# Kernel optimization log

Hardware: AMD Instinct MI355X
Metric: run time of the kernel (lower is better)

The kernel has to match this reference:

```python
import jax, jax.numpy as jnp
import numpy as np

B, T, D, H = 2, 2048, 1024, 16
HD = D // H            # head dim = 64
WINDOW = 512           # sliding-window size
EPS = 1e-6
ROPE_BASE = 10000.0


def setup_inputs() -> dict:
    key = jax.random.key(0)
    ks = jax.random.split(key, 5)
    s = 0.02  # init scale for dense kernels
    return {
        "x": jax.random.normal(ks[0], (B, T, D), jnp.float32),
        "Wq": jax.random.normal(ks[1], (D, D), jnp.float32) * s,
        "Wk": jax.random.normal(ks[2], (D, D), jnp.float32) * s,
        "Wv": jax.random.normal(ks[3], (D, D), jnp.float32) * s,
        "Wo": jax.random.normal(ks[4], (D, D), jnp.float32) * s,
        "q_scale": jnp.ones((HD,), jnp.float32),
        "k_scale": jnp.ones((HD,), jnp.float32),
        "sink_logit": jnp.zeros((H,), jnp.float32),
    }


def _rmsnorm(x, scale):
    # x: [..., HD]
    var = jnp.mean(jnp.square(x), axis=-1, keepdims=True)
    return x * jax.lax.rsqrt(var + EPS) * scale


def _rope(x):
    # x: [B, H, T, HD]; standard rotate-half RoPE over the full head dim
    half = HD // 2
    inv_freq = 1.0 / (ROPE_BASE ** (jnp.arange(0, HD, 2, dtype=jnp.float32) / HD))  # [half]
    t = jnp.arange(T, dtype=jnp.float32)
    freqs = t[:, None] * inv_freq[None, :]                # [T, half]
    emb = jnp.concatenate([freqs, freqs], axis=-1)        # [T, HD]
    cos = jnp.cos(emb)[None, None]                        # [1,1,T,HD]
    sin = jnp.sin(emb)[None, None]
    x1, x2 = x[..., :half], x[..., half:]
    rot = jnp.concatenate([-x2, x1], axis=-1)
    return x * cos + rot * sin


def reference(x, Wq, Wk, Wv, Wo, q_scale, k_scale, sink_logit):
    # projections -> [B, T, H, HD]
    q = (x @ Wq).reshape(B, T, H, HD)
    k = (x @ Wk).reshape(B, T, H, HD)
    v = (x @ Wv).reshape(B, T, H, HD)
    # QK RMSNorm over head dim
    q = _rmsnorm(q, q_scale)
    k = _rmsnorm(k, k_scale)
    # -> [B, H, T, HD], then RoPE
    q = _rope(q.transpose(0, 2, 1, 3))
    k = _rope(k.transpose(0, 2, 1, 3))
    v = v.transpose(0, 2, 1, 3)
    # causal sliding-window mask
    idx = jnp.arange(T)
    rel = idx[None, :] - idx[:, None]                     # key - query
    mask = ((rel <= 0) & (rel > -WINDOW))[None, None]     # [1,1,T,T]
    scale = HD ** (-0.5)
    scores = jnp.einsum('bhtd,bhsd->bhts', q, k) * scale
    scores = jnp.where(mask, scores, -jnp.inf)
    # sink-augmented softmax: append per-head sink logit to denominator
    sink = jnp.broadcast_to(sink_logit.reshape(1, H, 1, 1), (B, H, T, 1))
    aug = jnp.concatenate([scores.astype(jnp.float32), sink.astype(jnp.float32)], axis=-1)
    weights = jax.nn.softmax(aug, axis=-1)[..., :T].astype(scores.dtype)
    out = jnp.einsum('bhts,bhsd->bhtd', weights, v)
    out = out.transpose(0, 2, 1, 3).reshape(B, T, D)
    return out @ Wo
```

## Files before the change

### kernel.cpp

```cpp
#include <hip/hip_runtime.h>
#include <math.h>

#define CB 2
#define CT 2048
#define CD 1024
#define CH 16
#define CHD 64
#define CWINDOW 512

typedef __bf16 bf16x8 __attribute__((ext_vector_type(8)));
typedef float floatx4 __attribute__((ext_vector_type(4)));

__device__ __forceinline__ unsigned short f2bf(float f) {
  union { float f; unsigned int u; } v;
  v.f = f;
  unsigned int u = v.u;
  u += 0x7fffu + ((u >> 16) & 1u);
  return (unsigned short)(u >> 16);
}
__device__ __forceinline__ float bf2f(unsigned int h) {
  union { unsigned int u; float f; } v;
  v.u = h << 16;
  return v.f;
}

__global__ __launch_bounds__(256) void cvt_all(const float* __restrict__ x,
                                               const float* __restrict__ Wq,
                                               const float* __restrict__ Wk,
                                               const float* __restrict__ Wv,
                                               const float* __restrict__ Wo,
                                               unsigned short* __restrict__ xb,
                                               unsigned short* __restrict__ WqT,
                                               unsigned short* __restrict__ WkT,
                                               unsigned short* __restrict__ WvT,
                                               unsigned short* __restrict__ WoT) {
  const int z = blockIdx.z;
  if (z < 4) {
    const float* W = z == 0 ? Wq : z == 1 ? Wk : z == 2 ? Wv : Wo;
    unsigned short* Wt = z == 0 ? WqT : z == 1 ? WkT : z == 2 ? WvT : WoT;
    __shared__ float tile[64][65];
    const int k0 = blockIdx.x * 64, n0 = blockIdx.y * 64;
    const int c = threadIdx.x & 63, r4 = threadIdx.x >> 6;
#pragma unroll
    for (int i = 0; i < 16; ++i) {
      int r = i * 4 + r4;
      tile[r][c] = W[(size_t)(k0 + r) * CD + n0 + c];
    }
    __syncthreads();
#pragma unroll
    for (int i = 0; i < 16; ++i) {
      int r = i * 4 + r4;
      Wt[(size_t)(n0 + r) * CD + k0 + c] = f2bf(tile[c][r]);
    }
  } else {
    const int idx = (z - 4) * 256 + blockIdx.y * 16 + blockIdx.x;
    const int i = idx * 256 + threadIdx.x;
    float4 a = ((const float4*)x)[i * 2];
    float4 b = ((const float4*)x)[i * 2 + 1];
    uint4 o;
    o.x = (unsigned int)f2bf(a.x) | ((unsigned int)f2bf(a.y) << 16);
    o.y = (unsigned int)f2bf(a.z) | ((unsigned int)f2bf(a.w) << 16);
    o.z = (unsigned int)f2bf(b.x) | ((unsigned int)f2bf(b.y) << 16);
    o.w = (unsigned int)f2bf(b.z) | ((unsigned int)f2bf(b.w) << 16);
    ((uint4*)xb)[i] = o;
  }
}

__device__ __forceinline__ void async16(const unsigned short* g, unsigned short* l) {
  __builtin_amdgcn_global_load_lds(
      (const __attribute__((address_space(1))) unsigned int*)g,
      (__attribute__((address_space(3))) unsigned int*)l, 16, 0, 0);
}

template <int MODE, int BM>
__device__ __forceinline__ void mfma_gemm_body(const unsigned short* __restrict__ A,
                                               const unsigned short* __restrict__ Bt,
                                               void* __restrict__ Cout,
                                               const float* __restrict__ scale,
                                               float oscale) {
  constexpr int K = CD;
  constexpr int MT = BM / 32;
  __shared__ unsigned short As[BM * 32];
  __shared__ unsigned short Bs[128 * 32];
  const int tid = threadIdx.x;
  const int wave = tid >> 6, lane = tid & 63;
  const int m0 = blockIdx.x * BM, n0 = blockIdx.y * 128;
  const int mq = (wave & 1) * (BM / 2), nq = (wave >> 1) * 64;

  floatx4 acc[MT][4] = {};
  const int srow = lane >> 2;
  const int skc = (lane & 3) * 8;
  const int fr = lane & 15;
  const int fk = (lane >> 4) * 8;

  for (int k0 = 0; k0 < K; k0 += 32) {
    __syncthreads();
#pragma unroll
    for (int it = 0; it < BM / 64; ++it) {
      const int sub = wave * (BM / 64) + it;
      const int row = sub * 16 + srow;
      async16(A + (size_t)(m0 + row) * K + k0 + skc, &As[sub * 512]);
    }
#pragma unroll
    for (int it = 0; it < 2; ++it) {
      const int sub = wave * 2 + it;
      const int row = sub * 16 + srow;
      async16(Bt + (size_t)(n0 + row) * K + k0 + skc, &Bs[sub * 512]);
    }
    __syncthreads();
    bf16x8 af[MT], bg[4];
#pragma unroll
    for (int mt = 0; mt < MT; ++mt)
      af[mt] = *(const bf16x8*)&As[(mq + mt * 16 + fr) * 32 + fk];
#pragma unroll
    for (int nt = 0; nt < 4; ++nt)
      bg[nt] = *(const bf16x8*)&Bs[(nq + nt * 16 + fr) * 32 + fk];
#pragma unroll
    for (int mt = 0; mt < MT; ++mt)
#pragma unroll
      for (int nt = 0; nt < 4; ++nt)
        acc[mt][nt] = __builtin_amdgcn_mfma_f32_16x16x32_bf16(af[mt], bg[nt], acc[mt][nt], 0, 0, 0);
  }

  if (MODE == 1) {
    const int c = lane & 15, g = lane >> 4;
    const int hh = (n0 + nq) >> 6;
    const float kf = -0.2878231366242557f;
    const float inv0 = __expf((float)c * kf);
    const float inv1 = __expf((float)(16 + c) * kf);
    float sc[4];
#pragma unroll
    for (int nt = 0; nt < 4; ++nt) sc[nt] = scale[nt * 16 + c];
#pragma unroll
    for (int mt = 0; mt < MT; ++mt) {
#pragma unroll
      for (int i = 0; i < 4; ++i) {
        const int m = m0 + mq + mt * 16 + g * 4 + i;
        const int b = m >> 11, t = m & (CT - 1);
        float v0 = acc[mt][0][i], v1 = acc[mt][1][i];
        float v2 = acc[mt][2][i], v3 = acc[mt][3][i];
        float ss = v0 * v0 + v1 * v1 + v2 * v2 + v3 * v3;
#pragma unroll
        for (int off = 8; off > 0; off >>= 1) ss += __shfl_xor(ss, off);
        const float rs = rsqrtf(ss * (1.0f / 64.0f) + 1e-6f);
        v0 *= rs * sc[0];
        v1 *= rs * sc[1];
        v2 *= rs * sc[2];
        v3 *= rs * sc[3];
        const float tf = (float)t;
        const float a0 = tf * inv0, a1 = tf * inv1;
        const float s0 = __sinf(a0), c0 = __cosf(a0);
        const float s1 = __sinf(a1), c1 = __cosf(a1);
        unsigned short* dst = (unsigned short*)Cout + ((size_t)(b * CH + hh) * CT + t) * CHD;
        dst[c] = f2bf((v0 * c0 - v2 * s0) * oscale);
        dst[16 + c] = f2bf((v1 * c1 - v3 * s1) * oscale);
        dst[32 + c] = f2bf((v2 * c0 + v0 * s0) * oscale);
        dst[48 + c] = f2bf((v3 * c1 + v1 * s1) * oscale);
      }
    }
  } else {
#pragma unroll
    for (int mt = 0; mt < MT; ++mt) {
#pragma unroll
      for (int nt = 0; nt < 4; ++nt) {
        const int col = n0 + nq + nt * 16 + (lane & 15);
        if (MODE == 2) {
          const int mb = m0 + mq + mt * 16 + (lane >> 4) * 4;
          const int b = mb >> 11, t = mb & (CT - 1);
          const int h = col >> 6, d = col & 63;
          ushort4 o;
          o.x = f2bf(acc[mt][nt][0]);
          o.y = f2bf(acc[mt][nt][1]);
          o.z = f2bf(acc[mt][nt][2]);
          o.w = f2bf(acc[mt][nt][3]);
          *(ushort4*)&((unsigned short*)Cout)[((size_t)(b * CH + h) * CHD + d) * CT + t] = o;
        } else {
#pragma unroll
          for (int i = 0; i < 4; ++i) {
            const int m = m0 + mq + mt * 16 + (lane >> 4) * 4 + i;
            ((float*)Cout)[(size_t)m * CD + col] = acc[mt][nt][i];
          }
        }
      }
    }
  }
}

__global__ __launch_bounds__(256, 3) void gemm_qkv_mfma(const unsigned short* __restrict__ xb,
                                                        const unsigned short* __restrict__ WqT,
                                                        const unsigned short* __restrict__ WkT,
                                                        const unsigned short* __restrict__ WvT,
                                                        unsigned short* __restrict__ Qh,
                                                        unsigned short* __restrict__ Kh,
                                                        unsigned short* __restrict__ Vt,
                                                        const float* __restrict__ q_scale,
                                                        const float* __restrict__ k_scale) {
  if (blockIdx.z == 2) {
    mfma_gemm_body<2, 128>(xb, WvT, Vt, nullptr, 1.0f);
  } else if (blockIdx.z == 0) {
    mfma_gemm_body<1, 128>(xb, WqT, Qh, q_scale, 0.125f);
  } else {
    mfma_gemm_body<1, 128>(xb, WkT, Kh, k_scale, 1.0f);
  }
}

__global__ __launch_bounds__(256, 3) void gemm_out_mfma(const unsigned short* __restrict__ AO,
                                                        const unsigned short* __restrict__ WoT,
                                                        float* __restrict__ out) {
  mfma_gemm_body<0, 64>(AO, WoT, out, nullptr, 1.0f);
}

__device__ __forceinline__ bf16x8 frag64(const unsigned short* base, int row, int ks, int lane) {
  const int phys = (((ks << 2) + (lane >> 4)) ^ (lane & 7)) << 3;
  return *(const bf16x8*)&base[(row << 6) + phys];
}

__global__ __launch_bounds__(256, 2) void attn_mfma(const unsigned short* __restrict__ Qh,
                                                    const unsigned short* __restrict__ Kh,
                                                    const unsigned short* __restrict__ Vt,
                                                    const float* __restrict__ sink_logit,
                                                    unsigned short* __restrict__ AO) {
  __shared__ unsigned short Qs[128 * 64];
  __shared__ unsigned short Ks[64 * 64];
  __shared__ unsigned short Vs[64 * 64];
  __shared__ unsigned short Ps[128 * 72];

  const int tid = threadIdx.x;
  const int w = tid >> 6, lane = tid & 63;
  const int qb = blockIdx.x, bh = blockIdx.y;
  const int b = bh >> 4, h = bh & 15;
  const int q0 = qb * 128;
  const unsigned short* Qb = Qh + (size_t)bh * CT * CHD;
  const unsigned short* Kb = Kh + (size_t)bh * CT * CHD;
  const unsigned short* Vb = Vt + (size_t)bh * CHD * CT;

  const int l7 = lane & 7, l8 = lane >> 3;
  const int sx8 = (l7 ^ l8) * 8;

#pragma unroll
  for (int s = 0; s < 4; ++s) {
    const int slab = w * 4 + s;
    async16(Qb + (size_t)(q0 + slab * 8 + l8) * CHD + sx8, &Qs[slab * 512]);
  }
  __syncthreads();
  bf16x8 qf[2][2];
#pragma unroll
  for (int nt = 0; nt < 2; ++nt)
#pragma unroll
    for (int ks = 0; ks < 2; ++ks)
      qf[nt][ks] = frag64(Qs, w * 32 + nt * 16 + (lane & 15), ks, lane);

  floatx4 acc[4][2] = {};
  float lsum[2] = {0.f, 0.f};
  const int qw = q0 + w * 32;

  const int kb_lo = (qb >= 4) ? (qb * 2 - 8) : 0;
  const int kb_hi = qb * 2 + 1;
  for (int kb = kb_lo; kb <= kb_hi; ++kb) {
    __syncthreads();
#pragma unroll
    for (int s = 0; s < 2; ++s) {
      const int slab = w * 2 + s;
      const int row = slab * 8 + l8;
      async16(Kb + (size_t)(kb * 64 + row) * CHD + sx8, &Ks[slab * 512]);
      async16(Vb + (size_t)row * CT + kb * 64 + sx8, &Vs[slab * 512]);
    }
    __syncthreads();

    const int kmin = kb * 64, kmax = kb * 64 + 63;
    if (kmin > qw + 31 || kmax <= qw - CWINDOW) continue;

    floatx4 st[4][2] = {};
#pragma unroll
    for (int ks = 0; ks < 2; ++ks) {
      bf16x8 kf[4];
#pragma unroll
      for (int mt = 0; mt < 4; ++mt)
        kf[mt] = frag64(Ks, mt * 16 + (lane & 15), ks, lane);
#pragma unroll
      for (int mt = 0; mt < 4; ++mt)
#pragma unroll
        for (int nt = 0; nt < 2; ++nt)
          st[mt][nt] = __builtin_amdgcn_mfma_f32_16x16x32_bf16(kf[mt], qf[nt][ks], st[mt][nt], 0, 0, 0);
    }

    const bool need_c = (kmax > qw);
    const bool need_w = (kmin <= qw + 31 - CWINDOW);
#pragma unroll
    for (int mt = 0; mt < 4; ++mt) {
#pragma unroll
      for (int nt = 0; nt < 2; ++nt) {
        const int s_base = kb * 64 + mt * 16 + (lane >> 4) * 4;
        const int t_g = q0 + w * 32 + nt * 16 + (lane & 15);
        ushort4 pk;
        float psum = 0.f;
#pragma unroll
        for (int i = 0; i < 4; ++i) {
          float sv = st[mt][nt][i];
          if (need_c || need_w) {
            const int s_g = s_base + i;
            const bool ok = (!need_c || (s_g <= t_g)) && (!need_w || (s_g > t_g - CWINDOW));
            sv = ok ? sv : -INFINITY;
          }
          const float p = __expf(sv);
          const unsigned short pb = f2bf(p);
          ((unsigned short*)&pk)[i] = pb;
          psum += bf2f(pb);
        }
        lsum[nt] += psum;
        const int qrow = w * 32 + nt * 16 + (lane & 15);
        const int scol = mt * 16 + (lane >> 4) * 4;
        *(ushort4*)&Ps[qrow * 72 + scol] = pk;
      }
    }

#pragma unroll
    for (int ks = 0; ks < 2; ++ks) {
      bf16x8 vf[4], pf[2];
#pragma unroll
      for (int mt = 0; mt < 4; ++mt)
        vf[mt] = frag64(Vs, mt * 16 + (lane & 15), ks, lane);
#pragma unroll
      for (int nt = 0; nt < 2; ++nt) {
        const int qrow = w * 32 + nt * 16 + (lane & 15);
        pf[nt] = *(const bf16x8*)&Ps[qrow * 72 + ks * 32 + (lane >> 4) * 8];
      }
#pragma unroll
      for (int mt = 0; mt < 4; ++mt)
#pragma unroll
        for (int nt = 0; nt < 2; ++nt)
          acc[mt][nt] = __builtin_amdgcn_mfma_f32_16x16x32_bf16(vf[mt], pf[nt], acc[mt][nt], 0, 0, 0);
    }
  }

  const float sinkw = __expf(sink_logit[h]);
  float inv[2];
#pragma unroll
  for (int nt = 0; nt < 2; ++nt) {
    float l = lsum[nt];
    l += __shfl_xor(l, 16);
    l += __shfl_xor(l, 32);
    inv[nt] = 1.0f / (l + sinkw);
  }
#pragma unroll
  for (int mt = 0; mt < 4; ++mt) {
#pragma unroll
    for (int nt = 0; nt < 2; ++nt) {
      const int t_g = q0 + w * 32 + nt * 16 + (lane & 15);
      const int d0 = mt * 16 + (lane >> 4) * 4;
      ushort4 o;
      o.x = f2bf(acc[mt][nt][0] * inv[nt]);
      o.y = f2bf(acc[mt][nt][1] * inv[nt]);
      o.z = f2bf(acc[mt][nt][2] * inv[nt]);
      o.w = f2bf(acc[mt][nt][3] * inv[nt]);
      *(ushort4*)&AO[(size_t)(b * CT + t_g) * CD + h * CHD + d0] = o;
    }
  }
}

extern "C" void kernel_launch(void* const* d_in, const int* in_sizes, int n_in,
                              void* d_out, int out_size, void* d_ws, size_t ws_size,
                              hipStream_t stream) {
  (void)in_sizes;
  (void)n_in;
  (void)out_size;
  (void)ws_size;
  const float* x = (const float*)d_in[0];
  const float* Wq = (const float*)d_in[1];
  const float* Wk = (const float*)d_in[2];
  const float* Wv = (const float*)d_in[3];
  const float* Wo = (const float*)d_in[4];
  const float* q_scale = (const float*)d_in[5];
  const float* k_scale = (const float*)d_in[6];
  const float* sink = (const float*)d_in[7];
  float* out = (float*)d_out;

  const size_t per = (size_t)CB * CH * CT * CHD;
  unsigned short* Qh = (unsigned short*)d_ws;
  unsigned short* Kh = Qh + per;
  unsigned short* Vt = Kh + per;
  unsigned short* AO = Vt + per;
  unsigned short* xb = AO + per;
  unsigned short* WqT = xb + per;
  unsigned short* WkT = WqT + (size_t)CD * CD;
  unsigned short* WvT = WkT + (size_t)CD * CD;
  unsigned short* WoT = WvT + (size_t)CD * CD;

  dim3 blk(256);
  cvt_all<<<dim3(16, 16, 12), blk, 0, stream>>>(x, Wq, Wk, Wv, Wo, xb, WqT, WkT, WvT, WoT);
  gemm_qkv_mfma<<<dim3(32, 8, 3), blk, 0, stream>>>(xb, WqT, WkT, WvT, Qh, Kh, Vt, q_scale, k_scale);
  attn_mfma<<<dim3(CT / 128, CB * CH), blk, 0, stream>>>(Qh, Kh, Vt, sink, AO);
  gemm_out_mfma<<<dim3(64, 8), blk, 0, stream>>>(AO, WoT, out);
}
```

Before: 170.8 us.

## Double-buffer K/V tiles in attention and vectorize QK epilogue stores

The attention kernel now uses two LDS buffers for K and V. It issues the async loads for the next key block before computing on the current one, and keeps a single barrier per iteration instead of two. This is meant to hide global-to-LDS latency behind the MFMA and softmax work, at the cost of double the K/V shared memory, which could reduce occupancy. Separately, the Q/K projection epilogue packs its four bf16 outputs into one 8-byte store. This permutes the head-dim layout identically for Q and K, so the QK dot products stay the same.

New measurement: 169.1 us. About the same (-1.0%).

```diff
diff --git a/kernel.cpp b/kernel.cpp
--- a/kernel.cpp
+++ b/kernel.cpp
@@ -123,7 +123,8 @@
   }
 
   if (MODE == 1) {
-    const int c = lane & 15, g = lane >> 4;
+    const int c = lane & 15;
+    const int g = lane >> 4;
     const int hh = (n0 + nq) >> 6;
     const float kf = -0.2878231366242557f;
     const float inv0 = __expf((float)c * kf);
@@ -152,10 +153,12 @@
         const float s0 = __sinf(a0), c0 = __cosf(a0);
         const float s1 = __sinf(a1), c1 = __cosf(a1);
         unsigned short* dst = (unsigned short*)Cout + ((size_t)(b * CH + hh) * CT + t) * CHD;
-        dst[c] = f2bf((v0 * c0 - v2 * s0) * oscale);
-        dst[16 + c] = f2bf((v1 * c1 - v3 * s1) * oscale);
-        dst[32 + c] = f2bf((v2 * c0 + v0 * s0) * oscale);
-        dst[48 + c] = f2bf((v3 * c1 + v1 * s1) * oscale);
+        ushort4 o;
+        o.x = f2bf((v0 * c0 - v2 * s0) * oscale);
+        o.y = f2bf((v1 * c1 - v3 * s1) * oscale);
+        o.z = f2bf((v2 * c0 + v0 * s0) * oscale);
+        o.w = f2bf((v3 * c1 + v1 * s1) * oscale);
+        *(ushort4*)&dst[4 * c] = o;
       }
     }
   } else {
@@ -221,8 +224,8 @@
                                                     const float* __restrict__ sink_logit,
                                                     unsigned short* __restrict__ AO) {
   __shared__ unsigned short Qs[128 * 64];
-  __shared__ unsigned short Ks[64 * 64];
-  __shared__ unsigned short Vs[64 * 64];
+  __shared__ unsigned short Ks[2][64 * 64];
+  __shared__ unsigned short Vs[2][64 * 64];
   __shared__ unsigned short Ps[128 * 72];
 
   const int tid = threadIdx.x;
@@ -237,12 +240,26 @@
   const int l7 = lane & 7, l8 = lane >> 3;
   const int sx8 = (l7 ^ l8) * 8;
 
+  auto stageKV = [&](int bsel, int kb) {
+#pragma unroll
+    for (int s = 0; s < 2; ++s) {
+      const int slab = w * 2 + s;
+      const int row = slab * 8 + l8;
+      async16(Kb + (size_t)(kb * 64 + row) * CHD + sx8, &Ks[bsel][slab * 512]);
+      async16(Vb + (size_t)row * CT + kb * 64 + sx8, &Vs[bsel][slab * 512]);
+    }
+  };
+
 #pragma unroll
   for (int s = 0; s < 4; ++s) {
     const int slab = w * 4 + s;
     async16(Qb + (size_t)(q0 + slab * 8 + l8) * CHD + sx8, &Qs[slab * 512]);
   }
+  const int kb_lo = (qb >= 4) ? (qb * 2 - 8) : 0;
+  const int kb_hi = qb * 2 + 1;
+  stageKV(0, kb_lo);
   __syncthreads();
+
   bf16x8 qf[2][2];
 #pragma unroll
   for (int nt = 0; nt < 2; ++nt)
@@ -253,84 +270,81 @@
   floatx4 acc[4][2] = {};
   float lsum[2] = {0.f, 0.f};
   const int qw = q0 + w * 32;
-
-  const int kb_lo = (qb >= 4) ? (qb * 2 - 8) : 0;
-  const int kb_hi = qb * 2 + 1;
+  int buf = 0;
+
   for (int kb = kb_lo; kb <= kb_hi; ++kb) {
+    if (kb < kb_hi) stageKV(buf ^ 1, kb + 1);
+
+    const int kmin = kb * 64, kmax = kb * 64 + 63;
+    if (!(kmin > qw + 31 || kmax <= qw - CWINDOW)) {
+      const unsigned short* ksrc = Ks[buf];
+      const unsigned short* vsrc = Vs[buf];
+
+      floatx4 st[4][2] = {};
+#pragma unroll
+      for (int ks = 0; ks < 2; ++ks) {
+        bf16x8 kf[4];
+#pragma unroll
+        for (int mt = 0; mt < 4; ++mt)
+          kf[mt] = frag64(ksrc, mt * 16 + (lane & 15), ks, lane);
+#pragma unroll
+        for (int mt = 0; mt < 4; ++mt)
+#pragma unroll
+          for (int nt = 0; nt < 2; ++nt)
+            st[mt][nt] = __builtin_amdgcn_mfma_f32_16x16x32_bf16(kf[mt], qf[nt][ks], st[mt][nt], 0, 0, 0);
+      }
+
+      const bool need_c = (kmax > qw);
+      const bool need_w = (kmin <= qw + 31 - CWINDOW);
+#pragma unroll
+      for (int mt = 0; mt < 4; ++mt) {
+#pragma unroll
+        for (int nt = 0; nt < 2; ++nt) {
+          const int s_base = kb * 64 + mt * 16 + (lane >> 4) * 4;
+          const int t_g = q0 + w * 32 + nt * 16 + (lane & 15);
+          ushort4 pk;
+          float psum = 0.f;
+#pragma unroll
+          for (int i = 0; i < 4; ++i) {
+            float sv = st[mt][nt][i];
+            if (need_c || need_w) {
+              const int s_g = s_base + i;
+              const bool ok = (!need_c || (s_g <= t_g)) && (!need_w || (s_g > t_g - CWINDOW));
+              sv = ok ? sv : -INFINITY;
+            }
+            const float p = __expf(sv);
+            const unsigned short pb = f2bf(p);
+            ((unsigned short*)&pk)[i] = pb;
+            psum += bf2f(pb);
+          }
+          lsum[nt] += psum;
+          const int qrow = w * 32 + nt * 16 + (lane & 15);
+          const int scol = mt * 16 + (lane >> 4) * 4;
+          *(ushort4*)&Ps[qrow * 72 + scol] = pk;
+        }
+      }
+
+#pragma unroll
+      for (int ks = 0; ks < 2; ++ks) {
+        bf16x8 vf[4], pf[2];
+#pragma unroll
+        for (int mt = 0; mt < 4; ++mt)
+          vf[mt] = frag64(vsrc, mt * 16 + (lane & 15), ks, lane);
+#pragma unroll
+        for (int nt = 0; nt < 2; ++nt) {
+          const int qrow = w * 32 + nt * 16 + (lane & 15);
+          pf[nt] = *(const bf16x8*)&Ps[qrow * 72 + ks * 32 + (lane >> 4) * 8];
+        }
+#pragma unroll
+        for (int mt = 0; mt < 4; ++mt)
+#pragma unroll
+          for (int nt = 0; nt < 2; ++nt)
+            acc[mt][nt] = __builtin_amdgcn_mfma_f32_16x16x32_bf16(vf[mt], pf[nt], acc[mt][nt], 0, 0, 0);
+      }
+    }
+
+    buf ^= 1;
     __syncthreads();
-#pragma unroll
-    for (int s = 0; s < 2; ++s) {
-      const int slab = w * 2 + s;
-      const int row = slab * 8 + l8;
-      async16(Kb + (size_t)(kb * 64 + row) * CHD + sx8, &Ks[slab * 512]);
-      async16(Vb + (size_t)row * CT + kb * 64 + sx8, &Vs[slab * 512]);
-    }
-    __syncthreads();
-
-    const int kmin = kb * 64, kmax = kb * 64 + 63;
-    if (kmin > qw + 31 || kmax <= qw - CWINDOW) continue;
-
-    floatx4 st[4][2] = {};
-#pragma unroll
-    for (int ks = 0; ks < 2; ++ks) {
-      bf16x8 kf[4];
-#pragma unroll
-      for (int mt = 0; mt < 4; ++mt)
-        kf[mt] = frag64(Ks, mt * 16 + (lane & 15), ks, lane);
-#pragma unroll
-      for (int mt = 0; mt < 4; ++mt)
-#pragma unroll
-        for (int nt = 0; nt < 2; ++nt)
-          st[mt][nt] = __builtin_amdgcn_mfma_f32_16x16x32_bf16(kf[mt], qf[nt][ks], st[mt][nt], 0, 0, 0);
-    }
-
-    const bool need_c = (kmax > qw);
-    const bool need_w = (kmin <= qw + 31 - CWINDOW);
-#pragma unroll
-    for (int mt = 0; mt < 4; ++mt) {
-#pragma unroll
-      for (int nt = 0; nt < 2; ++nt) {
-        const int s_base = kb * 64 + mt * 16 + (lane >> 4) * 4;
-        const int t_g = q0 + w * 32 + nt * 16 + (lane & 15);
-        ushort4 pk;
-        float psum = 0.f;
-#pragma unroll
-        for (int i = 0; i < 4; ++i) {
-          float sv = st[mt][nt][i];
-          if (need_c || need_w) {
-            const int s_g = s_base + i;
-            const bool ok = (!need_c || (s_g <= t_g)) && (!need_w || (s_g > t_g - CWINDOW));
-            sv = ok ? sv : -INFINITY;
-          }
-          const float p = __expf(sv);
-          const unsigned short pb = f2bf(p);
-          ((unsigned short*)&pk)[i] = pb;
-          psum += bf2f(pb);
-        }
-        lsum[nt] += psum;
-        const int qrow = w * 32 + nt * 16 + (lane & 15);
-        const int scol = mt * 16 + (lane >> 4) * 4;
-        *(ushort4*)&Ps[qrow * 72 + scol] = pk;
-      }
-    }
-
-#pragma unroll
-    for (int ks = 0; ks < 2; ++ks) {
-      bf16x8 vf[4], pf[2];
-#pragma unroll
-      for (int mt = 0; mt < 4; ++mt)
-        vf[mt] = frag64(Vs, mt * 16 + (lane & 15), ks, lane);
-#pragma unroll
-      for (int nt = 0; nt < 2; ++nt) {
-        const int qrow = w * 32 + nt * 16 + (lane & 15);
-        pf[nt] = *(const bf16x8*)&Ps[qrow * 72 + ks * 32 + (lane >> 4) * 8];
-      }
-#pragma unroll
-      for (int mt = 0; mt < 4; ++mt)
-#pragma unroll
-        for (int nt = 0; nt < 2; ++nt)
-          acc[mt][nt] = __builtin_amdgcn_mfma_f32_16x16x32_bf16(vf[mt], pf[nt], acc[mt][nt], 0, 0, 0);
-    }
   }
 
   const float sinkw = __expf(sink_logit[h]);
```
